# Kernel optimization log

Hardware: AMD Instinct MI355X
Metric: run time of the kernel (lower is better)

Reference implementation:

```python
import jax, jax.numpy as jnp
import numpy as np

N0, N1, N2 = 100000, 25000, 6250
F = 128
OUT = 5


def _mean_agg(feat_src, src, dst, n_dst):
    # DGL copy_u + mean: segment mean over destination nodes (0 for isolated dst)
    s = jax.ops.segment_sum(feat_src[src], dst, num_segments=n_dst)
    cnt = jax.ops.segment_sum(jnp.ones_like(dst, dtype=feat_src.dtype), dst, num_segments=n_dst)
    return s / jnp.maximum(cnt, 1.0)[:, None]


def _graph_conv(feat, src, dst, W, b, n):
    # DGL GraphConv, norm='both': D_src^-1/2 gather-sum D_dst^-1/2, then linear
    dt = feat.dtype
    out_deg = jax.ops.segment_sum(jnp.ones_like(src, dtype=dt), src, num_segments=n)
    in_deg = jax.ops.segment_sum(jnp.ones_like(dst, dtype=dt), dst, num_segments=n)
    ns = jnp.where(out_deg > 0, out_deg ** -0.5, 0.0)
    nd = jnp.where(in_deg > 0, in_deg ** -0.5, 0.0)
    agg = jax.ops.segment_sum((feat * ns[:, None])[src], dst, num_segments=n)
    return (agg * nd[:, None]) @ W + b


def setup_inputs() -> dict:
    key = jax.random.key(0)
    keys = jax.random.split(key, 64)
    _c = iter(range(64))
    def nrm(shape, s=0.05):
        return jax.random.normal(keys[next(_c)], shape, dtype=jnp.float32) * s
    def ri(n, hi):
        return jax.random.randint(keys[next(_c)], (n,), 0, hi)
    inp = {
        'X': nrm((N0, 32), 1.0),
        'g0_src': ri(1600000, N0), 'g0_dst': ri(1600000, N0),
        'g1_src': ri(400000, N1), 'g1_dst': ri(400000, N1),
        'g2_src': ri(100000, N2), 'g2_dst': ri(100000, N2),
        'inc0_src': ri(100000, N0), 'inc0_dst': ri(100000, N1),
        'inc1_src': ri(25000, N1), 'inc1_dst': ri(25000, N2),
        'dec0_src': ri(100000, N2), 'dec0_dst': ri(100000, N1),
        'dec1_src': ri(400000, N1), 'dec1_dst': ri(400000, N0),
        'W_emb': nrm((32, F)), 'b_emb': jnp.zeros((F,), jnp.float32),
        'W_gcn0': nrm((F, F)), 'b_gcn0': jnp.zeros((F,), jnp.float32),
        'W_gcn1': nrm((F, F)), 'b_gcn1': jnp.zeros((F,), jnp.float32),
        'W_gcn2': nrm((F, F)), 'b_gcn2': jnp.zeros((F,), jnp.float32),
        'W_enc0': nrm((F, F)), 'b_enc0': jnp.zeros((F,), jnp.float32),
        'W_enc1': nrm((F, F)), 'b_enc1': jnp.zeros((F,), jnp.float32),
        'W_dec0': nrm((F, F)), 'b_dec0': jnp.zeros((F,), jnp.float32),
        'W_dec1': nrm((F, F)), 'b_dec1': jnp.zeros((F,), jnp.float32),
        'W_head0': nrm((2 * F, OUT)), 'b_head0': jnp.zeros((OUT,), jnp.float32),
        'W_head1': nrm((2 * F, OUT)), 'b_head1': jnp.zeros((OUT,), jnp.float32),
        'W_head2': nrm((2 * F, OUT)), 'b_head2': jnp.zeros((OUT,), jnp.float32),
    }
    return inp


def reference(X, g0_src, g0_dst, g1_src, g1_dst, g2_src, g2_dst,
              inc0_src, inc0_dst, inc1_src, inc1_dst,
              dec0_src, dec0_dst, dec1_src, dec1_dst,
              W_emb, b_emb, W_gcn0, b_gcn0, W_gcn1, b_gcn1, W_gcn2, b_gcn2,
              W_enc0, b_enc0, W_enc1, b_enc1, W_dec0, b_dec0, W_dec1, b_dec1,
              W_head0, b_head0, W_head1, b_head1, W_head2, b_head2):
    # embedding at finest scale
    h0 = X @ W_emb + b_emb                                   # [N0, F]
    # encode + pool fine -> coarse (copy_u/mean)
    h1 = _mean_agg(h0 @ W_enc0 + b_enc0, inc0_src, inc0_dst, N1)   # [N1, F]
    h2 = _mean_agg(h1 @ W_enc1 + b_enc1, inc1_src, inc1_dst, N2)   # [N2, F]
    # intra-scale GraphConv
    g0 = _graph_conv(h0, g0_src, g0_dst, W_gcn0, b_gcn0, N0)
    g1 = _graph_conv(h1, g1_src, g1_dst, W_gcn1, b_gcn1, N1)
    g2 = _graph_conv(h2, g2_src, g2_dst, W_gcn2, b_gcn2, N2)
    # decode coarse -> fine
    d2 = g2
    d1 = _mean_agg(d2 @ W_dec0 + b_dec0, dec0_src, dec0_dst, N1)   # [N1, F]
    d0 = _mean_agg(d1 @ W_dec1 + b_dec1, dec1_src, dec1_dst, N0)   # [N0, F]
    # per-scale heads with softmax
    o0 = jax.nn.softmax(jnp.concatenate([g0, d0], -1) @ W_head0 + b_head0, axis=-1)
    o1 = jax.nn.softmax(jnp.concatenate([g1, d1], -1) @ W_head1 + b_head1, axis=-1)
    o2 = jax.nn.softmax(jnp.concatenate([g2, d2], -1) @ W_head2 + b_head2, axis=-1)
    return jnp.concatenate([o0, o1, o2], axis=0)             # [N0+N1+N2, OUT]
```

## Files before the change

kernel.cpp:

```cpp
#include <hip/hip_runtime.h>

#define F 128
static const int N0 = 100000, N1 = 25000, N2 = 6250;

typedef unsigned short u16;
typedef unsigned int   u32;
typedef __attribute__((ext_vector_type(8))) short bf16x8;
typedef __attribute__((ext_vector_type(4))) float f32x4;

__device__ __forceinline__ float bf2f(u16 u) {
    union { u32 i; float f; } v; v.i = ((u32)u) << 16; return v.f;
}
__device__ __forceinline__ u16 f2bf(float f) {
    u32 u = __float_as_uint(f);
    u += 0x7fff + ((u >> 16) & 1);
    return (u16)(u >> 16);
}

struct Seg7 {
    const int* src[7];
    const int* dst[7];
    int end[7];
    int cbase[7];
    int obase[7];
};
struct W7 { const float* w[7]; };

#define EPT 4
#define CEPT 8
#define AST (F + 8)
#define SM32  (64*(32+8)*2 + 128*(32+8)*2 + 128*4)
#define SMA   (64*AST*2)


__device__ __forceinline__ void dev_mm32(char* smem, const float* __restrict__ Ap,
                                         const float* __restrict__ W,
                                         const float* __restrict__ bias,
                                         u16* __restrict__ out, int M, int blk) {
    const int K = 32;
    const int KST = K + 8;
    u16* Al = (u16*)smem;
    u16* Wt = (u16*)(smem + 64 * KST * 2);
    float* bl = (float*)(smem + 64 * KST * 2 + 128 * KST * 2);
    int tid = threadIdx.x;
    int m0 = blk * 64;

    for (int i = tid; i < K * 128; i += 256) {
        int k = i >> 7, n = i & 127;
        Wt[n * KST + k] = f2bf(W[i]);
    }
    for (int i = tid; i < 64 * K; i += 256) {
        int r = i / K, c = i % K;
        int gr = m0 + r;
        Al[r * KST + c] = (gr < M) ? f2bf(Ap[(size_t)gr * K + c]) : (u16)0;
    }
    if (tid < 128) bl[tid] = bias[tid];
    __syncthreads();

    int w = tid >> 6, lane = tid & 63, m16 = lane & 15, quad = lane >> 4;
    f32x4 acc[8];
#pragma unroll
    for (int t = 0; t < 8; t++)
#pragma unroll
        for (int r = 0; r < 4; r++) acc[t][r] = 0.f;

    for (int k0 = 0; k0 < K; k0 += 32) {
        bf16x8 af = *(const bf16x8*)&Al[(w * 16 + m16) * KST + k0 + quad * 8];
#pragma unroll
        for (int t = 0; t < 8; t++) {
            bf16x8 bf = *(const bf16x8*)&Wt[(t * 16 + m16) * KST + k0 + quad * 8];
            acc[t] = __builtin_amdgcn_mfma_f32_16x16x32_bf16(af, bf, acc[t], 0, 0, 0);
        }
    }
#pragma unroll
    for (int t = 0; t < 8; t++) {
#pragma unroll
        for (int r = 0; r < 4; r++) {
            int gr = m0 + w * 16 + quad * 4 + r;
            if (gr >= M) continue;
            int gc = t * 16 + m16;
            out[(size_t)gr * F + gc] = f2bf(acc[t][r] + bl[gc]);
        }
    }
}

template <bool MASK>
__device__ __forceinline__ void mfma128_core(const u16* Al,
                                             const u16* __restrict__ Wtg,
                                             const float* __restrict__ bias,
                                             u16* __restrict__ out,
                                             const int* __restrict__ rowptr,
                                             int M, int m0) {
    int tid = threadIdx.x;
    int wv = tid >> 6, lane = tid & 63, m16 = lane & 15, quad = lane >> 4;
    f32x4 acc[8];
#pragma unroll
    for (int t = 0; t < 8; t++)
#pragma unroll
        for (int r = 0; r < 4; r++) acc[t][r] = 0.f;

    for (int k0 = 0; k0 < F; k0 += 32) {
        bf16x8 af = *(const bf16x8*)&Al[(wv * 16 + m16) * AST + k0 + quad * 8];
#pragma unroll
        for (int t = 0; t < 8; t++) {
            bf16x8 bf = *(const bf16x8*)&Wtg[(t * 16 + m16) * F + k0 + quad * 8];
            acc[t] = __builtin_amdgcn_mfma_f32_16x16x32_bf16(af, bf, acc[t], 0, 0, 0);
        }
    }
#pragma unroll
    for (int t = 0; t < 8; t++) {
#pragma unroll
        for (int r = 0; r < 4; r++) {
            int gr = m0 + wv * 16 + quad * 4 + r;
            if (gr >= M) continue;
            int gc = t * 16 + m16;
            bool zrow = false;
            if (MASK) zrow = (rowptr[gr + 1] == rowptr[gr]);
            float v = acc[t][r] + bias[gc];
            out[(size_t)gr * F + gc] = zrow ? (u16)0 : f2bf(v);
        }
    }
}

template <bool MASK>
__device__ __forceinline__ void dev_mmd(char* smem, const u16* __restrict__ Ap,
                                        const u16* __restrict__ Wtg,
                                        const float* __restrict__ bias,
                                        u16* __restrict__ out,
                                        const int* __restrict__ rowptr,
                                        int M, int blk) {
    u16* Al = (u16*)smem;
    int tid = threadIdx.x;
    int m0 = blk * 64;
    for (int i = tid; i < 64 * F; i += 256) {
        int r = i >> 7, c = i & 127;
        int gr = m0 + r;
        Al[r * AST + c] = (gr < M) ? Ap[(size_t)gr * F + c] : (u16)0;
    }
    __syncthreads();
    mfma128_core<MASK>(Al, Wtg, bias, out, rowptr, M, m0);
}

template <int MODE, bool MASK, bool WRITEA>
__device__ __forceinline__ void dev_mmg(char* smem,
                                        const u16* __restrict__ feat,
                                        const int* __restrict__ rowptr,
                                        const int* __restrict__ col,
                                        const int* __restrict__ od,
                                        u16* __restrict__ Aout,
                                        const u16* __restrict__ Wtg,
                                        const float* __restrict__ bias,
                                        u16* __restrict__ out, int M, int blk) {
    u16* Al = (u16*)smem;
    int tid = threadIdx.x;
    int m0 = blk * 64;
    int wv = tid >> 6, lane = tid & 63;
    int fo = lane << 1;
    for (int r = wv; r < 64; r += 4) {
        int row = m0 + r;
        u16 x0 = 0, x1 = 0;
        if (row < M) {
            int beg = rowptr[row], end = rowptr[row + 1];
            float a0 = 0.f, a1 = 0.f;
            int j = beg;
            for (; j + 8 <= end; j += 8) {
                int cc[8];
#pragma unroll
                for (int t = 0; t < 8; t++) cc[t] = col[j + t];
                float ss[8];
#pragma unroll
                for (int t = 0; t < 8; t++) {
                    if (MODE == 1) { int o = od[cc[t]]; ss[t] = o > 0 ? rsqrtf((float)o) : 0.f; }
                    else ss[t] = 1.f;
                }
                ushort2 uu[8];
#pragma unroll
                for (int t = 0; t < 8; t++) uu[t] = *(const ushort2*)&feat[(size_t)cc[t] * F + fo];
#pragma unroll
                for (int t = 0; t < 8; t++) { a0 += bf2f(uu[t].x) * ss[t]; a1 += bf2f(uu[t].y) * ss[t]; }
            }
            for (; j < end; j++) {
                int c = col[j];
                float s = 1.f;
                if (MODE == 1) { int o = od[c]; s = o > 0 ? rsqrtf((float)o) : 0.f; }
                ushort2 u = *(const ushort2*)&feat[(size_t)c * F + fo];
                a0 += bf2f(u.x) * s; a1 += bf2f(u.y) * s;
            }
            int deg = end - beg;
            float fs = (MODE == 0) ? (deg > 0 ? 1.f / (float)deg : 0.f)
                                   : (deg > 0 ? rsqrtf((float)deg) : 0.f);
            x0 = f2bf(a0 * fs); x1 = f2bf(a1 * fs);
        }
        Al[r * AST + fo] = x0;
        Al[r * AST + fo + 1] = x1;
        if (WRITEA && row < M) {
            ushort2 o; o.x = x0; o.y = x1;
            *(ushort2*)&Aout[(size_t)row * F + fo] = o;
        }
    }
    __syncthreads();
    mfma128_core<MASK>(Al, Wtg, bias, out, rowptr, M, m0);
}

template <bool GD>
__device__ __forceinline__ void dev_head(char* smem, const u16* __restrict__ g,
                                         const u16* __restrict__ d,
                                         const int* __restrict__ rowptr,
                                         const int* __restrict__ col,
                                         const float* __restrict__ Wh,
                                         const float* __restrict__ bh,
                                         float* __restrict__ out, int M, int blk) {
    float* Wl = (float*)smem;
    float* bl = (float*)(smem + 1280 * 4);
    int tid = threadIdx.x;
    for (int i = tid; i < 1280; i += 256) Wl[i] = Wh[i];
    if (tid < 5) bl[tid] = bh[tid];
    __syncthreads();

    int lane = tid & 63;
    int wv = tid >> 6;
    int r0 = blk * 32 + wv * 8;
    int k0 = lane << 1;
    for (int i = 0; i < 8; i++) {
        int row = r0 + i;
        if (row < M) {
            float d0v, d1v;
            if (GD) {
                int beg = rowptr[row], end = rowptr[row + 1];
                d0v = 0.f; d1v = 0.f;
                int j = beg;
                for (; j + 4 <= end; j += 4) {
                    int c0 = col[j], c1 = col[j + 1], c2 = col[j + 2], c3 = col[j + 3];
                    ushort2 u0 = *(const ushort2*)&d[(size_t)c0 * F + k0];
                    ushort2 u1 = *(const ushort2*)&d[(size_t)c1 * F + k0];
                    ushort2 u2 = *(const ushort2*)&d[(size_t)c2 * F + k0];
                    ushort2 u3 = *(const ushort2*)&d[(size_t)c3 * F + k0];
                    d0v += bf2f(u0.x) + bf2f(u1.x) + bf2f(u2.x) + bf2f(u3.x);
                    d1v += bf2f(u0.y) + bf2f(u1.y) + bf2f(u2.y) + bf2f(u3.y);
                }
                for (; j < end; j++) {
                    int c = col[j];
                    ushort2 u = *(const ushort2*)&d[(size_t)c * F + k0];
                    d0v += bf2f(u.x); d1v += bf2f(u.y);
                }
                int deg = end - beg;
                float fs = deg > 0 ? 1.f / (float)deg : 0.f;
                d0v *= fs; d1v *= fs;
            } else {
                ushort2 du = *(const ushort2*)&d[(size_t)row * F + k0];
                d0v = bf2f(du.x); d1v = bf2f(du.y);
            }
            ushort2 gu = *(const ushort2*)&g[(size_t)row * F + k0];
            float g0v = bf2f(gu.x), g1v = bf2f(gu.y);
            float p[5];
#pragma unroll
            for (int o = 0; o < 5; o++) {
                p[o] = g0v * Wl[k0 * 5 + o] + g1v * Wl[(k0 + 1) * 5 + o] +
                       d0v * Wl[(k0 + 128) * 5 + o] + d1v * Wl[(k0 + 129) * 5 + o];
            }
#pragma unroll
            for (int o = 0; o < 5; o++) {
                float v = p[o];
                v += __shfl_xor(v, 32, 64);
                v += __shfl_xor(v, 16, 64);
                v += __shfl_xor(v, 8, 64);
                v += __shfl_xor(v, 4, 64);
                v += __shfl_xor(v, 2, 64);
                v += __shfl_xor(v, 1, 64);
                p[o] = v + bl[o];
            }
            if (lane == 0) {
                float m = p[0];
#pragma unroll
                for (int o = 1; o < 5; o++) m = fmaxf(m, p[o]);
                float e[5], s = 0.f;
#pragma unroll
                for (int o = 0; o < 5; o++) { e[o] = expf(p[o] - m); s += e[o]; }
                float inv = 1.f / s;
#pragma unroll
                for (int o = 0; o < 5; o++) out[(size_t)row * 5 + o] = e[o] * inv;
            }
        }
    }
}


__global__ __launch_bounds__(256) void k_count_emb(Seg7 S, W7 Wsrc,
                                                   u16* __restrict__ WtAll,
                                                   int* __restrict__ cnt,
                                                   u16* __restrict__ occ, int ETOT,
                                                   const float* __restrict__ X,
                                                   const float* __restrict__ Wemb,
                                                   const float* __restrict__ bemb,
                                                   u16* __restrict__ h0,
                                                   int nbMM, int nbPrep) {
    __shared__ char smem[SM32];
    int blk = blockIdx.x;
    if (blk < nbMM) {
        dev_mm32(smem, X, Wemb, bemb, h0, N0, blk);
        return;
    }
    if (blk < nbMM + nbPrep) {
        int g = (blk - nbMM) * 256 + threadIdx.x;
        int m = g >> 14, idx = g & 16383;
        int n = idx >> 7, k = idx & 127;
        WtAll[g] = f2bf(Wsrc.w[m][k * 128 + n]);
        return;
    }
    int base = (blk - nbMM - nbPrep) * (256 * CEPT) + threadIdx.x;
    int ee[CEPT], grow[CEPT];
#pragma unroll
    for (int t = 0; t < CEPT; t++) {
        int e = base + t * 256;
        ee[t] = e;
        grow[t] = -1;
        if (e < ETOT) {
            int s = 0;
            while (e >= S.end[s]) s++;
            int le = e - ((s == 0) ? 0 : S.end[s - 1]);
            grow[t] = S.cbase[s] + S.dst[s][le];
        }
    }
    u32 r[CEPT];
#pragma unroll
    for (int t = 0; t < CEPT; t++)
        if (grow[t] >= 0) r[t] = atomicAdd((u32*)&cnt[grow[t]], 1u);
#pragma unroll
    for (int t = 0; t < CEPT; t++)
        if (grow[t] >= 0) occ[ee[t]] = (u16)r[t];
}

__global__ __launch_bounds__(256) void k_fill_od(Seg7 S,
                                                 const int* __restrict__ rowptr,
                                                 const u16* __restrict__ occ,
                                                 int* __restrict__ col,
                                                 int* __restrict__ od, int ETOT,
                                                 float invRow, float invOd) {
    int win = blockIdx.x & 7;
    int base = ((int)blockIdx.x >> 3) * (256 * EPT) + threadIdx.x;
#pragma unroll
    for (int t = 0; t < EPT; t++) {
        int e = base + t * 256;
        if (e >= ETOT) break;
        int s = 0;
        while (e >= S.end[s]) s++;
        int le = e - ((s == 0) ? 0 : S.end[s - 1]);
        int grow = S.cbase[s] + S.dst[s][le];
        int w1 = (int)((float)grow * invRow); w1 = w1 > 7 ? 7 : w1;
        int sv = -1;
        if (w1 == win || S.obase[s] >= 0) sv = S.src[s][le];
        if (w1 == win) col[rowptr[grow] + (int)occ[e]] = sv;
        if (S.obase[s] >= 0) {
            int gs = S.obase[s] + sv;
            int w2 = (int)((float)gs * invOd); w2 = w2 > 7 ? 7 : w2;
            if (w2 == win) atomicAdd(&od[gs], 1);
        }
    }
}

#define SCHUNK 4096
__global__ __launch_bounds__(1024) void k_scan1(const int* __restrict__ cnt,
                                                int* __restrict__ partial, int n) {
    __shared__ int red[1024];
    int tid = threadIdx.x;
    int base = blockIdx.x * SCHUNK + tid * 4;
    int s = 0;
#pragma unroll
    for (int j = 0; j < 4; j++) { int i = base + j; if (i < n) s += cnt[i]; }
    red[tid] = s;
    __syncthreads();
    for (int d = 512; d > 0; d >>= 1) {
        if (tid < d) red[tid] += red[tid + d];
        __syncthreads();
    }
    if (tid == 0) partial[blockIdx.x] = red[0];
}

__global__ __launch_bounds__(128) void k_scan2(int* __restrict__ partial, int G) {
    __shared__ int sh[128];
    int tid = threadIdx.x;
    sh[tid] = (tid < G) ? partial[tid] : 0;
    __syncthreads();
    for (int d = 1; d < 128; d <<= 1) {
        int t = (tid >= d) ? sh[tid - d] : 0;
        __syncthreads();
        sh[tid] += t;
        __syncthreads();
    }
    if (tid < G) partial[tid] = (tid > 0) ? sh[tid - 1] : 0;
    if (tid == 127) partial[G] = sh[127];
}

__global__ __launch_bounds__(1024) void k_scan3(const int* __restrict__ cnt,
                                                const int* __restrict__ partial,
                                                int* __restrict__ rowptr,
                                                int n, int G) {
    __shared__ int red[1024];
    int tid = threadIdx.x;
    int base = blockIdx.x * SCHUNK + tid * 4;
    int v0 = 0, v1 = 0, v2 = 0, v3 = 0;
    if (base + 0 < n) v0 = cnt[base + 0];
    if (base + 1 < n) v1 = cnt[base + 1];
    if (base + 2 < n) v2 = cnt[base + 2];
    if (base + 3 < n) v3 = cnt[base + 3];
    red[tid] = v0 + v1 + v2 + v3;
    __syncthreads();
    for (int d = 1; d < 1024; d <<= 1) {
        int t = (tid >= d) ? red[tid - d] : 0;
        __syncthreads();
        red[tid] += t;
        __syncthreads();
    }
    int off = partial[blockIdx.x] + ((tid > 0) ? red[tid - 1] : 0);
    if (base + 0 < n) { rowptr[base + 0] = off; off += v0; }
    if (base + 1 < n) { rowptr[base + 1] = off; off += v1; }
    if (base + 2 < n) { rowptr[base + 2] = off; off += v2; }
    if (base + 3 < n) { rowptr[base + 3] = off; off += v3; }
    if (blockIdx.x == 0 && tid == 0) rowptr[n] = partial[G];
}

__global__ __launch_bounds__(256) void k_mmd(const u16* __restrict__ Ap,
                                             const u16* __restrict__ Wtg,
                                             const float* __restrict__ bias,
                                             u16* __restrict__ out, int M) {
    __shared__ char smem[SMA];
    dev_mmd<false>(smem, Ap, Wtg, bias, out, nullptr, M, blockIdx.x);
}

template <int MODE, bool MASK, bool WRITEA>
__global__ __launch_bounds__(256) void k_mmg(const u16* __restrict__ feat,
                                             const int* __restrict__ rowptr,
                                             const int* __restrict__ col,
                                             const int* __restrict__ od,
                                             u16* __restrict__ Aout,
                                             const u16* __restrict__ Wtg,
                                             const float* __restrict__ bias,
                                             u16* __restrict__ out, int M) {
    __shared__ char smem[SMA];
    dev_mmg<MODE, MASK, WRITEA>(smem, feat, rowptr, col, od, Aout, Wtg, bias, out, M, blockIdx.x);
}

__global__ __launch_bounds__(256) void k_mmg2(
    const u16* f1, const int* rp1, const u16* Wt1, const float* b1, u16* o1, int M1, int nb1,
    const u16* f2, const int* rp2, const int* od2, const u16* Wt2, const float* b2, u16* o2, int M2,
    const int* __restrict__ col) {
    __shared__ char smem[SMA];
    if ((int)blockIdx.x < nb1)
        dev_mmg<0, true, false>(smem, f1, rp1, col, nullptr, nullptr, Wt1, b1, o1, M1, blockIdx.x);
    else
        dev_mmg<1, false, false>(smem, f2, rp2, col, od2, nullptr, Wt2, b2, o2, M2, blockIdx.x - nb1);
}

__global__ __launch_bounds__(256) void k_head3(
    const u16* Ga, const u16* dFeat, const int* rpD1, const int* colp,
    const float* Wa, const float* Ba, int nb0,
    const u16* Gb, const u16* Db, const float* Wb, const float* Bb, int nb1,
    const u16* Gc, const float* Wc, const float* Bc,
    float* __restrict__ out) {
    __shared__ char smem[1280 * 4 + 32];
    int b = blockIdx.x;
    if (b < nb0)            dev_head<true >(smem, Ga, dFeat, rpD1, colp, Wa, Ba, out, N0, b);
    else if (b < nb0 + nb1) dev_head<false>(smem, Gb, Db, nullptr, nullptr, Wb, Bb, out + (size_t)N0 * 5, N1, b - nb0);
    else                    dev_head<false>(smem, Gc, Gc, nullptr, nullptr, Wc, Bc, out + (size_t)(N0 + N1) * 5, N2, b - nb0 - nb1);
}

extern "C" void kernel_launch(void* const* d_in, const int* in_sizes, int n_in,
                              void* d_out, int out_size, void* d_ws, size_t ws_size,
                              hipStream_t stream) {
    const float* X = (const float*)d_in[0];
    const int *g0s = (const int*)d_in[1], *g0d = (const int*)d_in[2];
    const int *g1s = (const int*)d_in[3], *g1d = (const int*)d_in[4];
    const int *g2s = (const int*)d_in[5], *g2d = (const int*)d_in[6];
    const int *i0s = (const int*)d_in[7], *i0d = (const int*)d_in[8];
    const int *i1s = (const int*)d_in[9], *i1d = (const int*)d_in[10];
    const int *dc0s = (const int*)d_in[11], *dc0d = (const int*)d_in[12];
    const int *dc1s = (const int*)d_in[13], *dc1d = (const int*)d_in[14];
    const float *Wemb = (const float*)d_in[15], *bemb = (const float*)d_in[16];
    const float *Wg0 = (const float*)d_in[17], *bg0 = (const float*)d_in[18];
    const float *Wg1 = (const float*)d_in[19], *bg1 = (const float*)d_in[20];
    const float *Wg2 = (const float*)d_in[21], *bg2 = (const float*)d_in[22];
    const float *We0 = (const float*)d_in[23], *be0 = (const float*)d_in[24];
    const float *We1 = (const float*)d_in[25], *be1 = (const float*)d_in[26];
    const float *Wd0 = (const float*)d_in[27], *bd0 = (const float*)d_in[28];
    const float *Wd1 = (const float*)d_in[29], *bd1 = (const float*)d_in[30];
    const float *Wh0 = (const float*)d_in[31], *bh0 = (const float*)d_in[32];
    const float *Wh1 = (const float*)d_in[33], *bh1 = (const float*)d_in[34];
    const float *Wh2 = (const float*)d_in[35], *bh2 = (const float*)d_in[36];
    const int Eg0 = in_sizes[1], Eg1 = in_sizes[3], Eg2 = in_sizes[5];
    const int Ei0 = in_sizes[7], Ei1 = in_sizes[9];
    const int Ed0 = in_sizes[11], Ed1 = in_sizes[13];
    (void)n_in; (void)out_size; (void)ws_size;

    const int B_I0 = 0;
    const int B_I1 = B_I0 + N1;
    const int B_G2 = B_I1 + N2;
    const int B_D0 = B_G2 + N2;
    const int B_G1 = B_D0 + N1;
    const int B_G0 = B_G1 + N1;
    const int B_D1 = B_G0 + N0;
    const int NROWS = B_D1 + N0;
    const int ETOT  = Eg0 + Eg1 + Eg2 + Ei0 + Ei1 + Ed0 + Ed1;
    const int OB_G0 = 0, OB_G1 = N0, OB_G2 = N0 + N1;
    const int NOD = N0 + N1 + N2;
    const int G = (NROWS + SCHUNK - 1) / SCHUNK;
    const int rowsPerWin = (NROWS + 7) / 8;
    const int odPerWin   = (NOD + 7) / 8;
    const float invRow = 1.0f / (float)rowsPerWin;
    const float invOd  = 1.0f / (float)odPerWin;
    const int NCH = (ETOT + 256 * EPT - 1) / (256 * EPT);

    char* wsb = (char*)d_ws;
    size_t off = 0;
    auto alloc = [&](size_t bytes) -> char* {
        char* p = wsb + off;
        off = (off + bytes + 255) & ~(size_t)255;
        return p;
    };
    u16* h0  = (u16*)alloc((size_t)N0 * F * 2);
    u16* h1  = (u16*)alloc((size_t)N1 * F * 2);
    u16* h2  = (u16*)alloc((size_t)N2 * F * 2);
    u16* G0  = (u16*)alloc((size_t)N0 * F * 2);
    u16* G1  = (u16*)alloc((size_t)N1 * F * 2);
    u16* G2  = (u16*)alloc((size_t)N2 * F * 2);
    u16* D1  = (u16*)alloc((size_t)N1 * F * 2);
    u16* bN1 = (u16*)alloc((size_t)N1 * F * 2);
    u16* bN2 = (u16*)alloc((size_t)N2 * F * 2);
    u16* WtAll = (u16*)alloc((size_t)7 * 16384 * 2);
    int* cnt    = (int*)alloc((size_t)NROWS * 4);
    int* od     = (int*)alloc((size_t)NOD * 4);
    int* rowptr = (int*)alloc((size_t)(NROWS + 1) * 4);
    u16* occ    = (u16*)alloc((size_t)ETOT * 2);
    int* col    = (int*)alloc((size_t)ETOT * 4);
    int* part   = (int*)alloc((size_t)(G + 1) * 4);
    float* out = (float*)d_out;

    u16* WtE0 = WtAll + 0 * 16384;
    u16* WtG0 = WtAll + 1 * 16384;
    u16* WtE1 = WtAll + 2 * 16384;
    u16* WtG1 = WtAll + 3 * 16384;
    u16* WtG2 = WtAll + 4 * 16384;
    u16* WtD0 = WtAll + 5 * 16384;
    u16* WtD1 = WtAll + 6 * 16384;
    W7 Wsrc;
    Wsrc.w[0] = We0; Wsrc.w[1] = Wg0; Wsrc.w[2] = We1; Wsrc.w[3] = Wg1;
    Wsrc.w[4] = Wg2; Wsrc.w[5] = Wd0; Wsrc.w[6] = Wd1;

    Seg7 S;
    S.src[0] = i0s;  S.dst[0] = i0d;  S.cbase[0] = B_I0; S.obase[0] = -1;
    S.src[1] = i1s;  S.dst[1] = i1d;  S.cbase[1] = B_I1; S.obase[1] = -1;
    S.src[2] = g2s;  S.dst[2] = g2d;  S.cbase[2] = B_G2; S.obase[2] = OB_G2;
    S.src[3] = dc0s; S.dst[3] = dc0d; S.cbase[3] = B_D0; S.obase[3] = -1;
    S.src[4] = g1s;  S.dst[4] = g1d;  S.cbase[4] = B_G1; S.obase[4] = OB_G1;
    S.src[5] = g0s;  S.dst[5] = g0d;  S.cbase[5] = B_G0; S.obase[5] = OB_G0;
    S.src[6] = dc1s; S.dst[6] = dc1d; S.cbase[6] = B_D1; S.obase[6] = -1;
    {
        int Es[7] = {Ei0, Ei1, Eg2, Ed0, Eg1, Eg0, Ed1};
        int acc = 0;
        for (int i = 0; i < 7; i++) { acc += Es[i]; S.end[i] = acc; }
    }

    const int nbEmb   = (N0 + 63) / 64;
    const int nbPrep  = (7 * 16384) / 256;
    const int nbCount = (ETOT + 256 * CEPT - 1) / (256 * CEPT);
    const int nbFill  = NCH * 8;

    hipMemsetAsync(cnt, 0, (size_t)((char*)od - (char*)cnt) + (size_t)NOD * 4, stream);
    k_count_emb<<<nbEmb + nbPrep + nbCount, 256, 0, stream>>>(
        S, Wsrc, WtAll, cnt, occ, ETOT, X, Wemb, bemb, h0, nbEmb, nbPrep);
    k_scan1<<<G, 1024, 0, stream>>>(cnt, part, NROWS);
    k_scan2<<<1, 128, 0, stream>>>(part, G);
    k_scan3<<<G, 1024, 0, stream>>>(cnt, part, rowptr, NROWS, G);
    k_fill_od<<<nbFill, 256, 0, stream>>>(S, rowptr, occ, col, od, ETOT, invRow, invOd);

    {
        int nb1 = (N1 + 63) / 64, nb2 = (N0 + 63) / 64;
        k_mmg2<<<nb1 + nb2, 256, 0, stream>>>(h0, rowptr + B_I0, WtE0, be0, h1, N1, nb1,
                                              h0, rowptr + B_G0, od + OB_G0, WtG0, bg0, G0, N0, col);
    }
    {
        int nb1 = (N2 + 63) / 64, nb2 = (N1 + 63) / 64;
        k_mmg2<<<nb1 + nb2, 256, 0, stream>>>(h1, rowptr + B_I1, WtE1, be1, h2, N2, nb1,
                                              h1, rowptr + B_G1, od + OB_G1, WtG1, bg1, G1, N1, col);
    }
    k_mmg<1, false, false><<<(N2 + 63) / 64, 256, 0, stream>>>(
        h2, rowptr + B_G2, col, od + OB_G2, nullptr, WtG2, bg2, G2, N2);
    k_mmd<<<(N2 + 63) / 64, 256, 0, stream>>>(G2, WtD0, bd0, bN2, N2);
    k_mmg<0, false, true><<<(N1 + 63) / 64, 256, 0, stream>>>(
        bN2, rowptr + B_D0, col, nullptr, D1, WtD1, bd1, bN1, N1);
    {
        int nb0 = (N0 + 31) / 32, nb1 = (N1 + 31) / 32, nb2 = (N2 + 31) / 32;
        k_head3<<<nb0 + nb1 + nb2, 256, 0, stream>>>(G0, bN1, rowptr + B_D1, col, Wh0, bh0, nb0,
                                                     G1, D1, Wh1, bh1, nb1,
                                                     G2, Wh2, bh2, out);
    }
}
```

Measured before the change: 822.8 us.

## Split fused gather+matmul kernels into separate gather and direct-load MFMA kernels

```diff
diff --git a/kernel.cpp b/kernel.cpp
--- a/kernel.cpp
+++ b/kernel.cpp
@@ -28,9 +28,7 @@
 
 #define EPT 4
 #define CEPT 8
-#define AST (F + 8)
 #define SM32  (64*(32+8)*2 + 128*(32+8)*2 + 128*4)
-#define SMA   (64*AST*2)
 
 
 __device__ __forceinline__ void dev_mm32(char* smem, const float* __restrict__ Ap,
@@ -64,11 +62,11 @@
 #pragma unroll
         for (int r = 0; r < 4; r++) acc[t][r] = 0.f;
 
-    for (int k0 = 0; k0 < K; k0 += 32) {
-        bf16x8 af = *(const bf16x8*)&Al[(w * 16 + m16) * KST + k0 + quad * 8];
+    {
+        bf16x8 af = *(const bf16x8*)&Al[(w * 16 + m16) * KST + quad * 8];
 #pragma unroll
         for (int t = 0; t < 8; t++) {
-            bf16x8 bf = *(const bf16x8*)&Wt[(t * 16 + m16) * KST + k0 + quad * 8];
+            bf16x8 bf = *(const bf16x8*)&Wt[(t * 16 + m16) * KST + quad * 8];
             acc[t] = __builtin_amdgcn_mfma_f32_16x16x32_bf16(af, bf, acc[t], 0, 0, 0);
         }
     }
@@ -85,22 +83,28 @@
 }
 
 template <bool MASK>
-__device__ __forceinline__ void mfma128_core(const u16* Al,
-                                             const u16* __restrict__ Wtg,
-                                             const float* __restrict__ bias,
-                                             u16* __restrict__ out,
-                                             const int* __restrict__ rowptr,
-                                             int M, int m0) {
+__device__ __forceinline__ void dev_mmd(const u16* __restrict__ Ap,
+                                        const u16* __restrict__ Wtg,
+                                        const float* __restrict__ bias,
+                                        u16* __restrict__ out,
+                                        const int* __restrict__ rowptr,
+                                        int M, int blk) {
     int tid = threadIdx.x;
     int wv = tid >> 6, lane = tid & 63, m16 = lane & 15, quad = lane >> 4;
+    int m0 = blk * 64;
+    int arow = m0 + wv * 16 + m16;
+    if (arow >= M) arow = M - 1;
+    const u16* Arow = Ap + (size_t)arow * F;
+
     f32x4 acc[8];
 #pragma unroll
     for (int t = 0; t < 8; t++)
 #pragma unroll
         for (int r = 0; r < 4; r++) acc[t][r] = 0.f;
 
+#pragma unroll
     for (int k0 = 0; k0 < F; k0 += 32) {
-        bf16x8 af = *(const bf16x8*)&Al[(wv * 16 + m16) * AST + k0 + quad * 8];
+        bf16x8 af = *(const bf16x8*)&Arow[k0 + quad * 8];
 #pragma unroll
         for (int t = 0; t < 8; t++) {
             bf16x8 bf = *(const bf16x8*)&Wtg[(t * 16 + m16) * F + k0 + quad * 8];
@@ -122,84 +126,47 @@
     }
 }
 
-template <bool MASK>
-__device__ __forceinline__ void dev_mmd(char* smem, const u16* __restrict__ Ap,
-                                        const u16* __restrict__ Wtg,
-                                        const float* __restrict__ bias,
-                                        u16* __restrict__ out,
-                                        const int* __restrict__ rowptr,
-                                        int M, int blk) {
-    u16* Al = (u16*)smem;
-    int tid = threadIdx.x;
-    int m0 = blk * 64;
-    for (int i = tid; i < 64 * F; i += 256) {
-        int r = i >> 7, c = i & 127;
-        int gr = m0 + r;
-        Al[r * AST + c] = (gr < M) ? Ap[(size_t)gr * F + c] : (u16)0;
-    }
-    __syncthreads();
-    mfma128_core<MASK>(Al, Wtg, bias, out, rowptr, M, m0);
-}
-
-template <int MODE, bool MASK, bool WRITEA>
-__device__ __forceinline__ void dev_mmg(char* smem,
-                                        const u16* __restrict__ feat,
-                                        const int* __restrict__ rowptr,
-                                        const int* __restrict__ col,
-                                        const int* __restrict__ od,
-                                        u16* __restrict__ Aout,
-                                        const u16* __restrict__ Wtg,
-                                        const float* __restrict__ bias,
-                                        u16* __restrict__ out, int M, int blk) {
-    u16* Al = (u16*)smem;
-    int tid = threadIdx.x;
-    int m0 = blk * 64;
-    int wv = tid >> 6, lane = tid & 63;
+template <int MODE>
+__device__ __forceinline__ void dev_gather(const u16* __restrict__ feat,
+                                           const int* __restrict__ rowptr,
+                                           const int* __restrict__ col,
+                                           const int* __restrict__ od,
+                                           u16* __restrict__ out, int M, int blk) {
+    int wv = (blk * 256 + (int)threadIdx.x) >> 6;
+    if (wv >= M) return;
+    int lane = threadIdx.x & 63;
     int fo = lane << 1;
-    for (int r = wv; r < 64; r += 4) {
-        int row = m0 + r;
-        u16 x0 = 0, x1 = 0;
-        if (row < M) {
-            int beg = rowptr[row], end = rowptr[row + 1];
-            float a0 = 0.f, a1 = 0.f;
-            int j = beg;
-            for (; j + 8 <= end; j += 8) {
-                int cc[8];
-#pragma unroll
-                for (int t = 0; t < 8; t++) cc[t] = col[j + t];
-                float ss[8];
-#pragma unroll
-                for (int t = 0; t < 8; t++) {
-                    if (MODE == 1) { int o = od[cc[t]]; ss[t] = o > 0 ? rsqrtf((float)o) : 0.f; }
-                    else ss[t] = 1.f;
-                }
-                ushort2 uu[8];
-#pragma unroll
-                for (int t = 0; t < 8; t++) uu[t] = *(const ushort2*)&feat[(size_t)cc[t] * F + fo];
-#pragma unroll
-                for (int t = 0; t < 8; t++) { a0 += bf2f(uu[t].x) * ss[t]; a1 += bf2f(uu[t].y) * ss[t]; }
-            }
-            for (; j < end; j++) {
-                int c = col[j];
-                float s = 1.f;
-                if (MODE == 1) { int o = od[c]; s = o > 0 ? rsqrtf((float)o) : 0.f; }
-                ushort2 u = *(const ushort2*)&feat[(size_t)c * F + fo];
-                a0 += bf2f(u.x) * s; a1 += bf2f(u.y) * s;
-            }
-            int deg = end - beg;
-            float fs = (MODE == 0) ? (deg > 0 ? 1.f / (float)deg : 0.f)
-                                   : (deg > 0 ? rsqrtf((float)deg) : 0.f);
-            x0 = f2bf(a0 * fs); x1 = f2bf(a1 * fs);
-        }
-        Al[r * AST + fo] = x0;
-        Al[r * AST + fo + 1] = x1;
-        if (WRITEA && row < M) {
-            ushort2 o; o.x = x0; o.y = x1;
-            *(ushort2*)&Aout[(size_t)row * F + fo] = o;
-        }
-    }
-    __syncthreads();
-    mfma128_core<MASK>(Al, Wtg, bias, out, rowptr, M, m0);
+    int beg = rowptr[wv], end = rowptr[wv + 1];
+    float a0 = 0.f, a1 = 0.f;
+    int j = beg;
+    for (; j + 8 <= end; j += 8) {
+        int cc[8];
+#pragma unroll
+        for (int t = 0; t < 8; t++) cc[t] = col[j + t];
+        float ss[8];
+#pragma unroll
+        for (int t = 0; t < 8; t++) {
+            if (MODE == 1) { int o = od[cc[t]]; ss[t] = o > 0 ? rsqrtf((float)o) : 0.f; }
+            else ss[t] = 1.f;
+        }
+        ushort2 uu[8];
+#pragma unroll
+        for (int t = 0; t < 8; t++) uu[t] = *(const ushort2*)&feat[(size_t)cc[t] * F + fo];
+#pragma unroll
+        for (int t = 0; t < 8; t++) { a0 += bf2f(uu[t].x) * ss[t]; a1 += bf2f(uu[t].y) * ss[t]; }
+    }
+    for (; j < end; j++) {
+        int c = col[j];
+        float s = 1.f;
+        if (MODE == 1) { int o = od[c]; s = o > 0 ? rsqrtf((float)o) : 0.f; }
+        ushort2 u = *(const ushort2*)&feat[(size_t)c * F + fo];
+        a0 += bf2f(u.x) * s; a1 += bf2f(u.y) * s;
+    }
+    int deg = end - beg;
+    float fs = (MODE == 0) ? (deg > 0 ? 1.f / (float)deg : 0.f)
+                           : (deg > 0 ? rsqrtf((float)deg) : 0.f);
+    ushort2 o; o.x = f2bf(a0 * fs); o.y = f2bf(a1 * fs);
+    *(ushort2*)&out[(size_t)wv * F + fo] = o;
 }
 
 template <bool GD>
@@ -419,36 +386,38 @@
     if (blockIdx.x == 0 && tid == 0) rowptr[n] = partial[G];
 }
 
+template <int MODE>
+__global__ __launch_bounds__(256) void k_gather(const u16* __restrict__ feat,
+                                                const int* __restrict__ rowptr,
+                                                const int* __restrict__ col,
+                                                const int* __restrict__ od,
+                                                u16* __restrict__ out, int M) {
+    dev_gather<MODE>(feat, rowptr, col, od, out, M, blockIdx.x);
+}
+
+template <int MA, int MB>
+__global__ __launch_bounds__(256) void k_gather2(
+    const u16* fA, const int* rpA, const int* oA, u16* outA, int MAr, int nbA,
+    const u16* fB, const int* rpB, const int* oB, u16* outB, int MBr,
+    const int* __restrict__ col) {
+    if ((int)blockIdx.x < nbA) dev_gather<MA>(fA, rpA, col, oA, outA, MAr, blockIdx.x);
+    else                       dev_gather<MB>(fB, rpB, col, oB, outB, MBr, blockIdx.x - nbA);
+}
+
+template <bool MASK>
 __global__ __launch_bounds__(256) void k_mmd(const u16* __restrict__ Ap,
                                              const u16* __restrict__ Wtg,
                                              const float* __restrict__ bias,
-                                             u16* __restrict__ out, int M) {
-    __shared__ char smem[SMA];
-    dev_mmd<false>(smem, Ap, Wtg, bias, out, nullptr, M, blockIdx.x);
-}
-
-template <int MODE, bool MASK, bool WRITEA>
-__global__ __launch_bounds__(256) void k_mmg(const u16* __restrict__ feat,
-                                             const int* __restrict__ rowptr,
-                                             const int* __restrict__ col,
-                                             const int* __restrict__ od,
-                                             u16* __restrict__ Aout,
-                                             const u16* __restrict__ Wtg,
-                                             const float* __restrict__ bias,
-                                             u16* __restrict__ out, int M) {
-    __shared__ char smem[SMA];
-    dev_mmg<MODE, MASK, WRITEA>(smem, feat, rowptr, col, od, Aout, Wtg, bias, out, M, blockIdx.x);
-}
-
-__global__ __launch_bounds__(256) void k_mmg2(
-    const u16* f1, const int* rp1, const u16* Wt1, const float* b1, u16* o1, int M1, int nb1,
-    const u16* f2, const int* rp2, const int* od2, const u16* Wt2, const float* b2, u16* o2, int M2,
-    const int* __restrict__ col) {
-    __shared__ char smem[SMA];
-    if ((int)blockIdx.x < nb1)
-        dev_mmg<0, true, false>(smem, f1, rp1, col, nullptr, nullptr, Wt1, b1, o1, M1, blockIdx.x);
-    else
-        dev_mmg<1, false, false>(smem, f2, rp2, col, od2, nullptr, Wt2, b2, o2, M2, blockIdx.x - nb1);
+                                             u16* __restrict__ out,
+                                             const int* __restrict__ rowptr, int M) {
+    dev_mmd<MASK>(Ap, Wtg, bias, out, rowptr, M, blockIdx.x);
+}
+
+__global__ __launch_bounds__(256) void k_mmd2(
+    const u16* A1, const u16* Wt1, const float* b1, u16* o1, const int* rp1, int M1, int nb1,
+    const u16* A2, const u16* Wt2, const float* b2, u16* o2, int M2) {
+    if ((int)blockIdx.x < nb1) dev_mmd<true >(A1, Wt1, b1, o1, rp1, M1, blockIdx.x);
+    else                       dev_mmd<false>(A2, Wt2, b2, o2, nullptr, M2, blockIdx.x - nb1);
 }
 
 __global__ __launch_bounds__(256) void k_head3(
@@ -523,8 +492,10 @@
     u16* G1  = (u16*)alloc((size_t)N1 * F * 2);
     u16* G2  = (u16*)alloc((size_t)N2 * F * 2);
     u16* D1  = (u16*)alloc((size_t)N1 * F * 2);
+    u16* agg = (u16*)alloc((size_t)N0 * F * 2);
     u16* bN1 = (u16*)alloc((size_t)N1 * F * 2);
     u16* bN2 = (u16*)alloc((size_t)N2 * F * 2);
+    u16* pA  = D1;
     u16* WtAll = (u16*)alloc((size_t)7 * 16384 * 2);
     int* cnt    = (int*)alloc((size_t)NROWS * 4);
     int* od     = (int*)alloc((size_t)NOD * 4);
@@ -573,20 +544,32 @@
     k_fill_od<<<nbFill, 256, 0, stream>>>(S, rowptr, occ, col, od, ETOT, invRow, invOd);
 
     {
+        int nbA = (N1 + 3) / 4, nbB = (N0 + 3) / 4;
+        k_gather2<0, 1><<<nbA + nbB, 256, 0, stream>>>(
+            h0, rowptr + B_I0, nullptr, pA, N1, nbA,
+            h0, rowptr + B_G0, od + OB_G0, agg, N0, col);
+    }
+    {
         int nb1 = (N1 + 63) / 64, nb2 = (N0 + 63) / 64;
-        k_mmg2<<<nb1 + nb2, 256, 0, stream>>>(h0, rowptr + B_I0, WtE0, be0, h1, N1, nb1,
-                                              h0, rowptr + B_G0, od + OB_G0, WtG0, bg0, G0, N0, col);
+        k_mmd2<<<nb1 + nb2, 256, 0, stream>>>(pA, WtE0, be0, h1, rowptr + B_I0, N1, nb1,
+                                              agg, WtG0, bg0, G0, N0);
+    }
+    {
+        int nbA = (N2 + 3) / 4, nbB = (N1 + 3) / 4;
+        k_gather2<0, 1><<<nbA + nbB, 256, 0, stream>>>(
+            h1, rowptr + B_I1, nullptr, bN2, N2, nbA,
+            h1, rowptr + B_G1, od + OB_G1, bN1, N1, col);
     }
     {
         int nb1 = (N2 + 63) / 64, nb2 = (N1 + 63) / 64;
-        k_mmg2<<<nb1 + nb2, 256, 0, stream>>>(h1, rowptr + B_I1, WtE1, be1, h2, N2, nb1,
-                                              h1, rowptr + B_G1, od + OB_G1, WtG1, bg1, G1, N1, col);
-    }
-    k_mmg<1, false, false><<<(N2 + 63) / 64, 256, 0, stream>>>(
-        h2, rowptr + B_G2, col, od + OB_G2, nullptr, WtG2, bg2, G2, N2);
-    k_mmd<<<(N2 + 63) / 64, 256, 0, stream>>>(G2, WtD0, bd0, bN2, N2);
-    k_mmg<0, false, true><<<(N1 + 63) / 64, 256, 0, stream>>>(
-        bN2, rowptr + B_D0, col, nullptr, D1, WtD1, bd1, bN1, N1);
+        k_mmd2<<<nb1 + nb2, 256, 0, stream>>>(bN2, WtE1, be1, h2, rowptr + B_I1, N2, nb1,
+                                              bN1, WtG1, bg1, G1, N1);
+    }
+    k_gather<1><<<(N2 + 3) / 4, 256, 0, stream>>>(h2, rowptr + B_G2, col, od + OB_G2, bN2, N2);
+    k_mmd<false><<<(N2 + 63) / 64, 256, 0, stream>>>(bN2, WtG2, bg2, G2, nullptr, N2);
+    k_mmd<false><<<(N2 + 63) / 64, 256, 0, stream>>>(G2, WtD0, bd0, bN2, nullptr, N2);
+    k_gather<0><<<(N1 + 3) / 4, 256, 0, stream>>>(bN2, rowptr + B_D0, col, nullptr, D1, N1);
+    k_mmd<false><<<(N1 + 63) / 64, 256, 0, stream>>>(D1, WtD1, bd1, bN1, nullptr, N1);
     {
         int nb0 = (N0 + 31) / 32, nb1 = (N1 + 31) / 32, nb2 = (N2 + 31) / 32;
         k_head3<<<nb0 + nb1 + nb2, 256, 0, stream>>>(G0, bN1, rowptr + B_D1, col, Wh0, bh0, nb0,
```

After: 691.9 us. 15.9% less time.
